# Optimization experiments

Measured on AMD Instinct MI355X. Metric: run time of the kernel, lower is better.

Reference implementation:

```python
import jax, jax.numpy as jnp
import numpy as np

WS = 7      # window size
SHIFT = 3   # shift size
H = 56
W = 56
NH = 16     # num heads


def _layernorm(x, g, b):
    m = x.mean(-1, keepdims=True)
    v = x.var(-1, keepdims=True)
    return (x - m) / jnp.sqrt(v + 1e-5) * g + b


def setup_inputs() -> dict:
    key = jax.random.key(0)
    ks = jax.random.split(key, 8)
    B, C = 16, 512
    DH = 4 * C
    s = 0.02
    x = jax.random.normal(ks[0], (B, H * W, C), jnp.float32)

    # relative position index (matches torch buffer construction)
    coords = np.stack(np.meshgrid(np.arange(WS), np.arange(WS), indexing='ij')).reshape(2, -1)
    rel = (coords[:, :, None] - coords[:, None, :]).transpose(1, 2, 0).copy()
    rel[..., 0] += WS - 1
    rel[..., 1] += WS - 1
    rel[..., 0] *= 2 * WS - 1
    rpi = jnp.asarray(rel.sum(-1), jnp.int32)  # (49, 49)

    # shifted-window additive attention mask (nW, N, N)
    img = np.zeros((H, W))
    cnt = 0
    for hs in (slice(0, -WS), slice(-WS, -SHIFT), slice(-SHIFT, None)):
        for wsl in (slice(0, -WS), slice(-WS, -SHIFT), slice(-SHIFT, None)):
            img[hs, wsl] = cnt
            cnt += 1
    mw = img.reshape(H // WS, WS, W // WS, WS).transpose(0, 2, 1, 3).reshape(-1, WS * WS)
    diff = mw[:, None, :] - mw[:, :, None]  # == mw.unsqueeze(1) - mw.unsqueeze(2)
    attn_mask = jnp.asarray(np.where(diff != 0, -100.0, 0.0), jnp.float32)

    return {
        'x': x,
        'rpi': rpi,
        'attn_mask': attn_mask,
        'norm1_g': jnp.ones((C,), jnp.float32),
        'norm1_b': jnp.zeros((C,), jnp.float32),
        'qkv_w': jax.random.normal(ks[1], (3 * C, C), jnp.float32) * s,
        'qkv_b': jnp.zeros((3 * C,), jnp.float32),
        'proj_w': jax.random.normal(ks[2], (C, C), jnp.float32) * s,
        'proj_b': jnp.zeros((C,), jnp.float32),
        'rpb_table': jax.random.normal(ks[3], ((2 * WS - 1) ** 2, NH), jnp.float32) * s,
        'norm2_g': jnp.ones((C,), jnp.float32),
        'norm2_b': jnp.zeros((C,), jnp.float32),
        'mlp_w1': jax.random.normal(ks[4], (DH, C), jnp.float32) * s,
        'mlp_b1': jnp.zeros((DH,), jnp.float32),
        'mlp_w2': jax.random.normal(ks[5], (C, DH), jnp.float32) * s,
        'mlp_b2': jnp.zeros((C,), jnp.float32),
    }


def reference(x, rpi, attn_mask, norm1_g, norm1_b, qkv_w, qkv_b, proj_w, proj_b,
              rpb_table, norm2_g, norm2_b, mlp_w1, mlp_b1, mlp_w2, mlp_b2):
    B, L, C = x.shape
    N = WS * WS
    nW = (H // WS) * (W // WS)
    hd = C // NH

    # --- attention branch ---
    h = _layernorm(x, norm1_g, norm1_b).reshape(B, H, W, C)
    h = jnp.roll(h, (-SHIFT, -SHIFT), axis=(1, 2))
    # window partition -> (B*nW, N, C)
    xw = h.reshape(B, H // WS, WS, W // WS, WS, C).transpose(0, 1, 3, 2, 4, 5).reshape(B * nW, N, C)

    qkv = (xw @ qkv_w.T + qkv_b).reshape(B * nW, N, 3, NH, hd).transpose(2, 0, 3, 1, 4)
    q, k, v = qkv[0], qkv[1], qkv[2]  # (B*nW, NH, N, hd)
    attn = jnp.einsum('bhnd,bhmd->bhnm', q * (hd ** -0.5), k)
    rpb = rpb_table[rpi].transpose(2, 0, 1)  # (NH, N, N)
    attn = attn + rpb[None]
    attn = attn.reshape(B, nW, NH, N, N) + attn_mask[None, :, None]
    attn = jax.nn.softmax(attn.reshape(B * nW, NH, N, N), axis=-1)
    o = jnp.einsum('bhnm,bhmd->bhnd', attn, v).transpose(0, 2, 1, 3).reshape(B * nW, N, C)
    o = o @ proj_w.T + proj_b
    # window reverse + unshift
    o = o.reshape(B, H // WS, W // WS, WS, WS, C).transpose(0, 1, 3, 2, 4, 5).reshape(B, H, W, C)
    o = jnp.roll(o, (SHIFT, SHIFT), axis=(1, 2)).reshape(B, L, C)

    x = x + o
    # --- MLP branch ---
    h2 = _layernorm(x, norm2_g, norm2_b)
    m = jax.nn.gelu(h2 @ mlp_w1.T + mlp_b1, approximate=False)
    return x + (m @ mlp_w2.T + mlp_b2)
```

## Files before the change

kernel.cpp:

```cpp
#include <hip/hip_runtime.h>
#include <hip/hip_bf16.h>

typedef __attribute__((ext_vector_type(8))) short bf16x8_t;
typedef __attribute__((ext_vector_type(4))) float f32x4_t;

__device__ __forceinline__ void gll16(const void* g, void* l) {
  __builtin_amdgcn_global_load_lds((const __attribute__((address_space(1))) void*)g,
                                   (__attribute__((address_space(3))) void*)l, 16, 0, 0);
}

__global__ __launch_bounds__(256) void k_cvt4(const float* __restrict__ s0, const float* __restrict__ s1,
                                              const float* __restrict__ s2, const float* __restrict__ s3,
                                              __hip_bfloat16* __restrict__ out) {
  int i4 = blockIdx.x * 256 + threadIdx.x;
  int i = i4 * 4;
  const float* src;
  int off;
  if (i < 786432)       { src = s0; off = i; }
  else if (i < 1048576) { src = s1; off = i - 786432; }
  else if (i < 2097152) { src = s2; off = i - 1048576; }
  else                  { src = s3; off = i - 2097152; }
  float4 v = *(const float4*)(src + off);
  union { __hip_bfloat16 h[4]; ushort2 u2[2]; } pk;
  pk.h[0] = __float2bfloat16(v.x); pk.h[1] = __float2bfloat16(v.y);
  pk.h[2] = __float2bfloat16(v.z); pk.h[3] = __float2bfloat16(v.w);
  *(ushort2*)(out + i) = pk.u2[0];
  *(ushort2*)(out + i + 2) = pk.u2[1];
}

__global__ __launch_bounds__(256) void k_cmb(const int* __restrict__ rpi,
                                             const float* __restrict__ tab,
                                             const float* __restrict__ mask,
                                             float* __restrict__ cmbp) {
  int idx = blockIdx.x * 256 + threadIdx.x;
  int jj = idx & 3, lane = (idx >> 2) & 63, tile = (idx >> 8) & 15;
  int h = (idx >> 12) & 15, w6 = idx >> 16;
  int r = (tile >> 2) * 16 + (lane >> 4) * 4 + jj;
  int c = (tile & 3) * 16 + (lane & 15);
  float v = -1e9f;
  if (r < 49 && c < 49) v = tab[rpi[r * 49 + c] * 16 + h] + mask[w6 * 2401 + r * 49 + c];
  cmbp[idx] = v;
}

template<int PERM>
__global__ __launch_bounds__(256) void k_ln(const float* __restrict__ in,
                                            const float* __restrict__ g,
                                            const float* __restrict__ bta,
                                            __hip_bfloat16* __restrict__ out) {
  const int w = threadIdx.x >> 6, l = threadIdx.x & 63;
  const int token = blockIdx.x * 4 + w;
  const float4* p = (const float4*)(in + (size_t)token * 512);
  float4 v0 = p[l], v1 = p[l + 64];
  float s  = v0.x + v0.y + v0.z + v0.w + v1.x + v1.y + v1.z + v1.w;
  float sq = v0.x*v0.x + v0.y*v0.y + v0.z*v0.z + v0.w*v0.w
           + v1.x*v1.x + v1.y*v1.y + v1.z*v1.z + v1.w*v1.w;
  #pragma unroll
  for (int d = 1; d < 64; d <<= 1) { s += __shfl_xor(s, d); sq += __shfl_xor(sq, d); }
  float mean = s * (1.f / 512.f);
  float inv = rsqrtf(sq * (1.f / 512.f) - mean * mean + 1e-5f);
  size_t dst;
  if (PERM) {
    int b = token / 3136, pp = token - b * 3136;
    int i = pp / 56, j = pp - i * 56;
    int gi = (i + 53) % 56, gj = (j + 53) % 56;
    dst = ((size_t)(((b * 64) + (gi / 7) * 8 + (gj / 7)) * 49) + (gi % 7) * 7 + (gj % 7)) * 512;
  } else {
    dst = (size_t)token * 512;
  }
  int c0 = l * 4, c1 = 256 + l * 4;
  union { __hip_bfloat16 h[4]; ushort4 u4; } a, b4;
  a.h[0] = __float2bfloat16((v0.x - mean) * inv * g[c0]     + bta[c0]);
  a.h[1] = __float2bfloat16((v0.y - mean) * inv * g[c0 + 1] + bta[c0 + 1]);
  a.h[2] = __float2bfloat16((v0.z - mean) * inv * g[c0 + 2] + bta[c0 + 2]);
  a.h[3] = __float2bfloat16((v0.w - mean) * inv * g[c0 + 3] + bta[c0 + 3]);
  b4.h[0] = __float2bfloat16((v1.x - mean) * inv * g[c1]     + bta[c1]);
  b4.h[1] = __float2bfloat16((v1.y - mean) * inv * g[c1 + 1] + bta[c1 + 1]);
  b4.h[2] = __float2bfloat16((v1.z - mean) * inv * g[c1 + 2] + bta[c1 + 2]);
  b4.h[3] = __float2bfloat16((v1.w - mean) * inv * g[c1 + 3] + bta[c1 + 3]);
  *(ushort4*)(out + dst + c0) = a.u4;
  *(ushort4*)(out + dst + c1) = b4.u4;
}

__global__ __launch_bounds__(256) void k_attn(const __hip_bfloat16* __restrict__ qkv,
                                              const float* __restrict__ cmbp,
                                              __hip_bfloat16* __restrict__ o) {
  __shared__ __align__(16) __hip_bfloat16 vt_all[4 * 32 * 72];
  __shared__ __align__(16) __hip_bfloat16 P_all[4 * 64 * 72];
  const int t = threadIdx.x, l = t & 63, w = t >> 6;
  const int bw = blockIdx.x;
  const int head = blockIdx.y * 4 + w;
  const int rr = l & 15, g = l >> 4;
  __hip_bfloat16* vt = vt_all + w * (32 * 72);
  __hip_bfloat16* P  = P_all  + w * (64 * 72);
  const __hip_bfloat16* base = qkv + (size_t)bw * 49 * 1536 + head * 32;
  const bf16x8_t zero8 = {};

  { int d = l >> 1, sg = (l & 1) * 8;
    *(bf16x8_t*)(vt + d * 72 + 48 + sg) = zero8; }
  __builtin_amdgcn_sched_barrier(0);
  #pragma unroll
  for (int it = 0; it < 4; ++it) {
    int idx = l + it * 64;
    if (idx < 196) {
      int j = idx >> 2, sg = (idx & 3) * 8;
      bf16x8_t vv = *(const bf16x8_t*)(base + 1024 + (size_t)j * 1536 + sg);
      #pragma unroll
      for (int s2 = 0; s2 < 8; ++s2) vt[(sg + s2) * 72 + j] = ((__hip_bfloat16*)&vv)[s2];
    }
  }
  bf16x8_t aq[4], bk[4];
  #pragma unroll
  for (int m = 0; m < 4; ++m) {
    int row = m * 16 + rr;
    aq[m] = (row < 49) ? *(const bf16x8_t*)(base + (size_t)row * 1536 + g * 8) : zero8;
    bk[m] = (row < 49) ? *(const bf16x8_t*)(base + 512 + (size_t)row * 1536 + g * 8) : zero8;
  }
  const float4* cp = (const float4*)(cmbp + (size_t)((bw & 63) * 16 + head) * 4096);
  f32x4_t S[4][4];
  #pragma unroll
  for (int tm = 0; tm < 4; ++tm)
    #pragma unroll
    for (int tn = 0; tn < 4; ++tn) {
      float4 cv = cp[(tm * 4 + tn) * 64 + l];
      f32x4_t c0 = { cv.x, cv.y, cv.z, cv.w };
      S[tm][tn] = __builtin_amdgcn_mfma_f32_16x16x32_bf16(aq[tm], bk[tn], c0, 0, 0, 0);
    }
  float sm[4][4];
  #pragma unroll
  for (int tm = 0; tm < 4; ++tm) {
    #pragma unroll
    for (int jj = 0; jj < 4; ++jj) {
      float v = fmaxf(fmaxf(S[tm][0][jj], S[tm][1][jj]), fmaxf(S[tm][2][jj], S[tm][3][jj]));
      v = fmaxf(v, __shfl_xor(v, 1));
      v = fmaxf(v, __shfl_xor(v, 2));
      v = fmaxf(v, __shfl_xor(v, 4));
      v = fmaxf(v, __shfl_xor(v, 8));
      float s = 0.f;
      #pragma unroll
      for (int tn = 0; tn < 4; ++tn) {
        float e = __expf(S[tm][tn][jj] - v);
        S[tm][tn][jj] = e;
        s += e;
      }
      s += __shfl_xor(s, 1); s += __shfl_xor(s, 2); s += __shfl_xor(s, 4); s += __shfl_xor(s, 8);
      sm[tm][jj] = s;
    }
  }
  #pragma unroll
  for (int tm = 0; tm < 4; ++tm)
    #pragma unroll
    for (int tn = 0; tn < 4; ++tn)
      #pragma unroll
      for (int jj = 0; jj < 4; ++jj)
        P[(tm * 16 + g * 4 + jj) * 72 + tn * 16 + rr] = __float2bfloat16(S[tm][tn][jj]);

  f32x4_t O[4][2] = {};
  #pragma unroll
  for (int ks = 0; ks < 2; ++ks) {
    bf16x8_t pa[4], vb[2];
    #pragma unroll
    for (int tm = 0; tm < 4; ++tm)
      pa[tm] = *(const bf16x8_t*)(P + (tm * 16 + rr) * 72 + ks * 32 + g * 8);
    #pragma unroll
    for (int tn = 0; tn < 2; ++tn)
      vb[tn] = *(const bf16x8_t*)(vt + (tn * 16 + rr) * 72 + ks * 32 + g * 8);
    #pragma unroll
    for (int tm = 0; tm < 4; ++tm)
      #pragma unroll
      for (int tn = 0; tn < 2; ++tn)
        O[tm][tn] = __builtin_amdgcn_mfma_f32_16x16x32_bf16(pa[tm], vb[tn], O[tm][tn], 0, 0, 0);
  }
  #pragma unroll
  for (int tm = 0; tm < 4; ++tm) {
    #pragma unroll
    for (int jj = 0; jj < 4; ++jj) {
      int r = tm * 16 + g * 4 + jj;
      if (r < 49) {
        float rcp = 1.f / sm[tm][jj];
        size_t ob = ((size_t)bw * 49 + r) * 512 + head * 32;
        o[ob + rr]      = __float2bfloat16(O[tm][0][jj] * rcp);
        o[ob + 16 + rr] = __float2bfloat16(O[tm][1][jj] * rcp);
      }
    }
  }
}

template<int EP>
__global__ __launch_bounds__(512, 2) void gemm256(const __hip_bfloat16* __restrict__ A,
                                                  const __hip_bfloat16* __restrict__ Bw,
                                                  int K, int Ncols, int nNB,
                                                  const float* __restrict__ bias,
                                                  __hip_bfloat16* __restrict__ obf,
                                                  const float* __restrict__ resid,
                                                  float* __restrict__ ofp) {
  __shared__ __align__(16) char LDS[131072];
  const int nwg = gridDim.x, orig = blockIdx.x;
  const int q8 = nwg >> 3, r8 = nwg & 7;
  const int xcd = orig & 7, lin = orig >> 3;
  const int wgid = (xcd < r8 ? xcd * (q8 + 1) : r8 * (q8 + 1) + (xcd - r8) * q8) + lin;
  const int bx = wgid / nNB, by = wgid - bx * nNB;
  const int m0 = bx * 256, n0 = by * 256;
  const int t = threadIdx.x, l = t & 63, w = t >> 6;
  const int wr = w >> 2, wc = w & 3;
  const int rr = l & 15, kq = l >> 4;
  const int swzo = (kq * 16) ^ ((rr & 8) << 2);

  int rs0, cs0, rs1, cs1;
  { int d = t * 16;  rs0 = (d >> 10) * 16 + ((d >> 6) & 15);
    cs0 = ((d & 63) ^ (((d >> 9) & 1) << 5)) >> 1; }
  { int d = 8192 + t * 16; int dd = d & 8191;
    rs1 = (dd >> 10) * 16 + ((dd >> 6) & 15);
    cs1 = 32 + (((d & 63) ^ (((d >> 9) & 1) << 5)) >> 1); }
  const __hip_bfloat16* gA = A + (size_t)m0 * K;
  const __hip_bfloat16* gB = Bw + (size_t)n0 * K;

  auto stageA = [&](int T, int h) {
    char* dst = LDS + (T & 1) * 32768 + h * 16384 + t * 16;
    const size_t kb = (size_t)T * 64;
    gll16(gA + (size_t)(h * 128 + rs0) * K + kb + cs0, dst);
    gll16(gA + (size_t)(h * 128 + rs1) * K + kb + cs1, dst + 8192);
  };
  auto stageB = [&](int T, int h) {
    char* dst = LDS + 65536 + (T & 1) * 32768 + h * 16384 + t * 16;
    const size_t kb = (size_t)T * 64;
    gll16(gB + (size_t)(h * 128 + rs0) * K + kb + cs0, dst);
    gll16(gB + (size_t)(h * 128 + rs1) * K + kb + cs1, dst + 8192);
  };

  auto ldA = [&](bf16x8_t (&a)[4][2], int buf, int mq) {
    const char* b = LDS + buf * 32768 + wr * 16384;
    #pragma unroll
    for (int m = 0; m < 4; ++m)
      #pragma unroll
      for (int ks = 0; ks < 2; ++ks)
        a[m][ks] = *(const bf16x8_t*)(b + ks * 8192 + (mq * 4 + m) * 1024 + rr * 64 + swzo);
  };
  auto ldB = [&](bf16x8_t (&bv)[2][2], int buf, int nq) {
    const char* b = LDS + 65536 + buf * 32768 + (wc >> 1) * 16384;
    #pragma unroll
    for (int n = 0; n < 2; ++n)
      #pragma unroll
      for (int ks = 0; ks < 2; ++ks)
        bv[n][ks] = *(const bf16x8_t*)(b + ks * 8192 + ((wc & 1) * 4 + nq * 2 + n) * 1024 + rr * 64 + swzo);
  };

  f32x4_t acc[8][4] = {};
  auto mma = [&](bf16x8_t (&a)[4][2], bf16x8_t (&bv)[2][2], int mq, int nq) {
    __builtin_amdgcn_s_setprio(1);
    #pragma unroll
    for (int m = 0; m < 4; ++m)
      #pragma unroll
      for (int n = 0; n < 2; ++n)
        #pragma unroll
        for (int ks = 0; ks < 2; ++ks)
          acc[mq * 4 + m][nq * 2 + n] =
            __builtin_amdgcn_mfma_f32_16x16x32_bf16(a[m][ks], bv[n][ks], acc[mq * 4 + m][nq * 2 + n], 0, 0, 0);
    __builtin_amdgcn_s_setprio(0);
  };

  const int NT = K >> 6;
  stageA(0, 0); stageB(0, 0); stageA(0, 1); stageB(0, 1);
  if (1 < NT) { stageA(1, 0); stageB(1, 0); }
  if (1 < NT) asm volatile("s_waitcnt vmcnt(4)" ::: "memory");
  else        asm volatile("s_waitcnt vmcnt(0)" ::: "memory");
  __builtin_amdgcn_s_barrier();

  for (int kt = 0; kt < NT; ++kt) {
    const int cur = kt & 1;
    bf16x8_t Alo[4][2], Ahi[4][2], B0[2][2], B1[2][2];
    ldA(Alo, cur, 0); ldB(B0, cur, 0);
    if (kt + 1 < NT) stageA(kt + 1, 1);
    mma(Alo, B0, 0, 0);
    ldA(Ahi, cur, 1);
    if (kt + 1 < NT) stageB(kt + 1, 1);
    mma(Ahi, B0, 1, 0);
    __builtin_amdgcn_s_barrier();
    ldB(B1, cur, 1);
    if (kt + 2 < NT) stageA(kt + 2, 0);
    mma(Ahi, B1, 1, 1);
    if (kt + 2 < NT) stageB(kt + 2, 0);
    mma(Alo, B1, 0, 1);
    if (kt + 1 < NT) {
      if (kt + 2 < NT) asm volatile("s_waitcnt vmcnt(4)" ::: "memory");
      else             asm volatile("s_waitcnt vmcnt(0)" ::: "memory");
    }
    __builtin_amdgcn_s_barrier();
  }

  #pragma unroll
  for (int m = 0; m < 8; ++m) {
    #pragma unroll
    for (int n = 0; n < 4; ++n) {
      const int gcol = n0 + wc * 64 + n * 16 + rr;
      #pragma unroll
      for (int j = 0; j < 4; ++j) {
        const int grow = m0 + wr * 128 + m * 16 + kq * 4 + j;
        float v = acc[m][n][j] + bias[gcol];
        if (EP == 0) {
          if (gcol < 512) v *= 0.17677669529663687f;
          obf[(size_t)grow * Ncols + gcol] = __float2bfloat16(v);
        } else if (EP == 1) {
          int bw = grow / 49, nn = grow - bw * 49;
          int b = bw >> 6, wi = bw & 63;
          int hh = (wi >> 3) * 7 + nn / 7 + 3;  if (hh >= 56) hh -= 56;
          int ww2 = (wi & 7) * 7 + (nn % 7) + 3; if (ww2 >= 56) ww2 -= 56;
          size_t tok = (size_t)b * 3136 + hh * 56 + ww2;
          ofp[tok * 512 + gcol] = resid[tok * 512 + gcol] + v;
        } else if (EP == 2) {
          float u = 0.5f * v * (1.f + erff(v * 0.70710678118f));
          obf[(size_t)grow * Ncols + gcol] = __float2bfloat16(u);
        } else {
          ofp[(size_t)grow * 512 + gcol] += v;
        }
      }
    }
  }
}

extern "C" void kernel_launch(void* const* d_in, const int* in_sizes, int n_in,
                              void* d_out, int out_size, void* d_ws, size_t ws_size,
                              hipStream_t stream) {
  const float* x      = (const float*)d_in[0];
  const int*   rpi    = (const int*)  d_in[1];
  const float* amask  = (const float*)d_in[2];
  const float* n1g    = (const float*)d_in[3];
  const float* n1b    = (const float*)d_in[4];
  const float* qkv_w  = (const float*)d_in[5];
  const float* qkv_b  = (const float*)d_in[6];
  const float* proj_w = (const float*)d_in[7];
  const float* proj_b = (const float*)d_in[8];
  const float* rpb_t  = (const float*)d_in[9];
  const float* n2g    = (const float*)d_in[10];
  const float* n2b    = (const float*)d_in[11];
  const float* w1     = (const float*)d_in[12];
  const float* b1     = (const float*)d_in[13];
  const float* w2     = (const float*)d_in[14];
  const float* b2     = (const float*)d_in[15];
  float* out = (float*)d_out;

  char* ws = (char*)d_ws;
  const size_t M = 50176;
  const size_t szA = M * 2048 * 2;
  const size_t szB = M * 1536 * 2;
  const size_t offB = szA;
  const size_t offW = offB + szB;
  __hip_bfloat16* bufA = (__hip_bfloat16*)(ws);
  __hip_bfloat16* bufB = (__hip_bfloat16*)(ws + offB);
  __hip_bfloat16* wqkv  = (__hip_bfloat16*)(ws + offW);
  float* cmbp = (float*)(ws + szA - (size_t)4194304 * 4);
  __hip_bfloat16* wproj = wqkv + 786432;
  __hip_bfloat16* wm1   = wproj + 262144;
  __hip_bfloat16* wm2   = wm1 + 1048576;

  k_cvt4<<<3072, 256, 0, stream>>>(qkv_w, proj_w, w1, w2, wqkv);
  k_cmb<<<16384, 256, 0, stream>>>(rpi, rpb_t, amask, cmbp);

  k_ln<1><<<12544, 256, 0, stream>>>(x, n1g, n1b, bufA);
  gemm256<0><<<196 * 6, 512, 0, stream>>>(bufA, wqkv, 512, 1536, 6, qkv_b, bufB, nullptr, nullptr);
  k_attn<<<dim3(1024, 4), 256, 0, stream>>>(bufB, cmbp, bufA);
  gemm256<1><<<196 * 2, 512, 0, stream>>>(bufA, wproj, 512, 512, 2, proj_b, nullptr, x, out);
  k_ln<0><<<12544, 256, 0, stream>>>(out, n2g, n2b, bufB);
  gemm256<2><<<196 * 8, 512, 0, stream>>>(bufB, wm1, 512, 2048, 8, b1, bufA, nullptr, nullptr);
  gemm256<3><<<196 * 2, 512, 0, stream>>>(bufA, wm2, 2048, 512, 2, b2, nullptr, nullptr, out);
}
```

Measured before the change: 761.9 us.

## Reshape GEMM tiles from 256x256 to 128x512 with a rebalanced staging schedule

Changes the GEMM block tile from 256x256 to 128 rows by 512 columns. Each of the eight waves now covers all 128 rows and a 64-column strip, and B is staged as four 128-row sub-tiles across a reworked double-buffered pipeline. For the N=512 projection and MLP-down GEMMs, a single column tile now covers the full output width, so A is read once and each row's epilogue index math (including the window-reverse scatter) is hoisted out of the column loop. In exchange, LDS grows to 160KB per block, which likely drops occupancy to one block per CU, and global load volume per output increases.

```diff
diff --git a/kernel.cpp b/kernel.cpp
--- a/kernel.cpp
+++ b/kernel.cpp
@@ -186,22 +186,21 @@
 }
 
 template<int EP>
-__global__ __launch_bounds__(512, 2) void gemm256(const __hip_bfloat16* __restrict__ A,
-                                                  const __hip_bfloat16* __restrict__ Bw,
-                                                  int K, int Ncols, int nNB,
-                                                  const float* __restrict__ bias,
-                                                  __hip_bfloat16* __restrict__ obf,
-                                                  const float* __restrict__ resid,
-                                                  float* __restrict__ ofp) {
-  __shared__ __align__(16) char LDS[131072];
+__global__ __launch_bounds__(512, 2) void gemm_w(const __hip_bfloat16* __restrict__ A,
+                                                 const __hip_bfloat16* __restrict__ Bw,
+                                                 int K, int Ncols, int nNB,
+                                                 const float* __restrict__ bias,
+                                                 __hip_bfloat16* __restrict__ obf,
+                                                 const float* __restrict__ resid,
+                                                 float* __restrict__ ofp) {
+  __shared__ __align__(16) char LDS[163840];
   const int nwg = gridDim.x, orig = blockIdx.x;
   const int q8 = nwg >> 3, r8 = nwg & 7;
   const int xcd = orig & 7, lin = orig >> 3;
   const int wgid = (xcd < r8 ? xcd * (q8 + 1) : r8 * (q8 + 1) + (xcd - r8) * q8) + lin;
   const int bx = wgid / nNB, by = wgid - bx * nNB;
-  const int m0 = bx * 256, n0 = by * 256;
+  const int m0 = bx * 128, n0 = by * 512;
   const int t = threadIdx.x, l = t & 63, w = t >> 6;
-  const int wr = w >> 2, wc = w & 3;
   const int rr = l & 15, kq = l >> 4;
   const int swzo = (kq * 16) ^ ((rr & 8) << 2);
 
@@ -214,34 +213,39 @@
   const __hip_bfloat16* gA = A + (size_t)m0 * K;
   const __hip_bfloat16* gB = Bw + (size_t)n0 * K;
 
-  auto stageA = [&](int T, int h) {
-    char* dst = LDS + (T & 1) * 32768 + h * 16384 + t * 16;
+  auto stageA = [&](int T) {
+    char* dst = LDS + (T & 1) * 16384 + t * 16;
     const size_t kb = (size_t)T * 64;
-    gll16(gA + (size_t)(h * 128 + rs0) * K + kb + cs0, dst);
-    gll16(gA + (size_t)(h * 128 + rs1) * K + kb + cs1, dst + 8192);
-  };
-  auto stageB = [&](int T, int h) {
-    char* dst = LDS + 65536 + (T & 1) * 32768 + h * 16384 + t * 16;
+    gll16(gA + (size_t)rs0 * K + kb + cs0, dst);
+    gll16(gA + (size_t)rs1 * K + kb + cs1, dst + 8192);
+  };
+  auto stageBu = [&](int T, int u) {
+    char* dst = LDS + 32768 + (T & 1) * 65536 + u * 16384 + t * 16;
     const size_t kb = (size_t)T * 64;
-    gll16(gB + (size_t)(h * 128 + rs0) * K + kb + cs0, dst);
-    gll16(gB + (size_t)(h * 128 + rs1) * K + kb + cs1, dst + 8192);
+    gll16(gB + (size_t)(u * 128 + rs0) * K + kb + cs0, dst);
+    gll16(gB + (size_t)(u * 128 + rs1) * K + kb + cs1, dst + 8192);
   };
 
   auto ldA = [&](bf16x8_t (&a)[4][2], int buf, int mq) {
-    const char* b = LDS + buf * 32768 + wr * 16384;
-    #pragma unroll
-    for (int m = 0; m < 4; ++m)
+    const char* b = LDS + buf * 16384;
+    #pragma unroll
+    for (int m = 0; m < 4; ++m) {
+      int r = mq * 64 + m * 16 + rr;
       #pragma unroll
       for (int ks = 0; ks < 2; ++ks)
-        a[m][ks] = *(const bf16x8_t*)(b + ks * 8192 + (mq * 4 + m) * 1024 + rr * 64 + swzo);
+        a[m][ks] = *(const bf16x8_t*)(b + ks * 8192 + (r >> 4) * 1024 + (r & 15) * 64 + swzo);
+    }
   };
   auto ldB = [&](bf16x8_t (&bv)[2][2], int buf, int nq) {
-    const char* b = LDS + 65536 + buf * 32768 + (wc >> 1) * 16384;
-    #pragma unroll
-    for (int n = 0; n < 2; ++n)
+    #pragma unroll
+    for (int n = 0; n < 2; ++n) {
+      int rB = w * 64 + (nq * 2 + n) * 16 + rr;
+      const char* b = LDS + 32768 + buf * 65536 + (rB >> 7) * 16384;
+      int r = rB & 127;
       #pragma unroll
       for (int ks = 0; ks < 2; ++ks)
-        bv[n][ks] = *(const bf16x8_t*)(b + ks * 8192 + ((wc & 1) * 4 + nq * 2 + n) * 1024 + rr * 64 + swzo);
+        bv[n][ks] = *(const bf16x8_t*)(b + ks * 8192 + (r >> 4) * 1024 + (r & 15) * 64 + swzo);
+    }
   };
 
   f32x4_t acc[8][4] = {};
@@ -259,30 +263,31 @@
   };
 
   const int NT = K >> 6;
-  stageA(0, 0); stageB(0, 0); stageA(0, 1); stageB(0, 1);
-  if (1 < NT) { stageA(1, 0); stageB(1, 0); }
+  stageA(0); stageBu(0, 0); stageBu(0, 1); stageBu(0, 2); stageBu(0, 3);
+  if (1 < NT) { stageBu(1, 0); stageBu(1, 1); }
   if (1 < NT) asm volatile("s_waitcnt vmcnt(4)" ::: "memory");
   else        asm volatile("s_waitcnt vmcnt(0)" ::: "memory");
   __builtin_amdgcn_s_barrier();
 
   for (int kt = 0; kt < NT; ++kt) {
     const int cur = kt & 1;
-    bf16x8_t Alo[4][2], Ahi[4][2], B0[2][2], B1[2][2];
-    ldA(Alo, cur, 0); ldB(B0, cur, 0);
-    if (kt + 1 < NT) stageA(kt + 1, 1);
-    mma(Alo, B0, 0, 0);
-    ldA(Ahi, cur, 1);
-    if (kt + 1 < NT) stageB(kt + 1, 1);
-    mma(Ahi, B0, 1, 0);
+    const bool nx1 = (kt + 1 < NT), nx2 = (kt + 2 < NT);
+    bf16x8_t Am0[4][2], Am1[4][2], Bn0[2][2], Bn1[2][2];
+    ldA(Am0, cur, 0); ldB(Bn0, cur, 0);
+    if (nx1) stageBu(kt + 1, 2);
+    mma(Am0, Bn0, 0, 0);
+    ldA(Am1, cur, 1); ldB(Bn1, cur, 1);
+    if (nx1) stageBu(kt + 1, 3);
+    mma(Am1, Bn0, 1, 0);
     __builtin_amdgcn_s_barrier();
-    ldB(B1, cur, 1);
-    if (kt + 2 < NT) stageA(kt + 2, 0);
-    mma(Ahi, B1, 1, 1);
-    if (kt + 2 < NT) stageB(kt + 2, 0);
-    mma(Alo, B1, 0, 1);
-    if (kt + 1 < NT) {
-      if (kt + 2 < NT) asm volatile("s_waitcnt vmcnt(4)" ::: "memory");
-      else             asm volatile("s_waitcnt vmcnt(0)" ::: "memory");
+    if (nx1) stageA(kt + 1);
+    if (nx2) stageBu(kt + 2, 0);
+    mma(Am1, Bn1, 1, 1);
+    if (nx2) stageBu(kt + 2, 1);
+    mma(Am0, Bn1, 0, 1);
+    if (nx1) {
+      if (nx2) asm volatile("s_waitcnt vmcnt(4)" ::: "memory");
+      else     asm volatile("s_waitcnt vmcnt(0)" ::: "memory");
     }
     __builtin_amdgcn_s_barrier();
   }
@@ -290,27 +295,34 @@
   #pragma unroll
   for (int m = 0; m < 8; ++m) {
     #pragma unroll
-    for (int n = 0; n < 4; ++n) {
-      const int gcol = n0 + wc * 64 + n * 16 + rr;
-      #pragma unroll
-      for (int j = 0; j < 4; ++j) {
-        const int grow = m0 + wr * 128 + m * 16 + kq * 4 + j;
+    for (int j = 0; j < 4; ++j) {
+      const int grow = m0 + m * 16 + kq * 4 + j;
+      size_t rowbase;
+      if (EP == 1) {
+        int bw = grow / 49, nn = grow - bw * 49;
+        int b = bw >> 6, wi = bw & 63;
+        int hh = (wi >> 3) * 7 + nn / 7 + 3;  if (hh >= 56) hh -= 56;
+        int ww2 = (wi & 7) * 7 + (nn % 7) + 3; if (ww2 >= 56) ww2 -= 56;
+        rowbase = ((size_t)b * 3136 + hh * 56 + ww2) * 512;
+      } else if (EP == 3) {
+        rowbase = (size_t)grow * 512;
+      } else {
+        rowbase = (size_t)grow * Ncols;
+      }
+      #pragma unroll
+      for (int n = 0; n < 4; ++n) {
+        const int gcol = n0 + w * 64 + n * 16 + rr;
         float v = acc[m][n][j] + bias[gcol];
         if (EP == 0) {
           if (gcol < 512) v *= 0.17677669529663687f;
-          obf[(size_t)grow * Ncols + gcol] = __float2bfloat16(v);
+          obf[rowbase + gcol] = __float2bfloat16(v);
         } else if (EP == 1) {
-          int bw = grow / 49, nn = grow - bw * 49;
-          int b = bw >> 6, wi = bw & 63;
-          int hh = (wi >> 3) * 7 + nn / 7 + 3;  if (hh >= 56) hh -= 56;
-          int ww2 = (wi & 7) * 7 + (nn % 7) + 3; if (ww2 >= 56) ww2 -= 56;
-          size_t tok = (size_t)b * 3136 + hh * 56 + ww2;
-          ofp[tok * 512 + gcol] = resid[tok * 512 + gcol] + v;
+          ofp[rowbase + gcol] = resid[rowbase + gcol] + v;
         } else if (EP == 2) {
           float u = 0.5f * v * (1.f + erff(v * 0.70710678118f));
-          obf[(size_t)grow * Ncols + gcol] = __float2bfloat16(u);
+          obf[rowbase + gcol] = __float2bfloat16(u);
         } else {
-          ofp[(size_t)grow * 512 + gcol] += v;
+          ofp[rowbase + gcol] += v;
         }
       }
     }
@@ -356,10 +368,10 @@
   k_cmb<<<16384, 256, 0, stream>>>(rpi, rpb_t, amask, cmbp);
 
   k_ln<1><<<12544, 256, 0, stream>>>(x, n1g, n1b, bufA);
-  gemm256<0><<<196 * 6, 512, 0, stream>>>(bufA, wqkv, 512, 1536, 6, qkv_b, bufB, nullptr, nullptr);
+  gemm_w<0><<<392 * 3, 512, 0, stream>>>(bufA, wqkv, 512, 1536, 3, qkv_b, bufB, nullptr, nullptr);
   k_attn<<<dim3(1024, 4), 256, 0, stream>>>(bufB, cmbp, bufA);
-  gemm256<1><<<196 * 2, 512, 0, stream>>>(bufA, wproj, 512, 512, 2, proj_b, nullptr, x, out);
+  gemm_w<1><<<392, 512, 0, stream>>>(bufA, wproj, 512, 512, 1, proj_b, nullptr, x, out);
   k_ln<0><<<12544, 256, 0, stream>>>(out, n2g, n2b, bufB);
-  gemm256<2><<<196 * 8, 512, 0, stream>>>(bufB, wm1, 512, 2048, 8, b1, bufA, nullptr, nullptr);
-  gemm256<3><<<196 * 2, 512, 0, stream>>>(bufA, wm2, 2048, 512, 2, b2, nullptr, nullptr, out);
-}
+  gemm_w<2><<<392 * 4, 512, 0, stream>>>(bufB, wm1, 512, 2048, 4, b1, bufA, nullptr, nullptr);
+  gemm_w<3><<<392, 512, 0, stream>>>(bufA, wm2, 2048, 512, 1, b2, nullptr, nullptr, out);
+}
```

New measurement: 777.6 us. 2.1% more time.

## Fuse projection GEMM with residual and LayerNorm2; split-K the second MLP GEMM

Applied to the files above, without the earlier changes.

A new kernel computes full 128x512 row tiles of the attention projection. In its epilogue it un-permutes rows back to token order, adds the residual, writes the fp32 output and applies LayerNorm2 to produce the bf16 MLP input. This removes the separate LayerNorm kernel and its extra pass over the activations. The final MLP GEMM is also split along K into two halves that atomically add into the output, doubling the number of workgroups for the 392-tile problem. The costs are a heavier epilogue with 160KB of LDS per block, which limits occupancy, plus fp32 atomic traffic and non-deterministic summation order.

```diff
diff --git a/kernel.cpp b/kernel.cpp
--- a/kernel.cpp
+++ b/kernel.cpp
@@ -42,11 +42,10 @@
   cmbp[idx] = v;
 }
 
-template<int PERM>
-__global__ __launch_bounds__(256) void k_ln(const float* __restrict__ in,
-                                            const float* __restrict__ g,
-                                            const float* __restrict__ bta,
-                                            __hip_bfloat16* __restrict__ out) {
+__global__ __launch_bounds__(256) void k_ln1(const float* __restrict__ in,
+                                             const float* __restrict__ g,
+                                             const float* __restrict__ bta,
+                                             __hip_bfloat16* __restrict__ out) {
   const int w = threadIdx.x >> 6, l = threadIdx.x & 63;
   const int token = blockIdx.x * 4 + w;
   const float4* p = (const float4*)(in + (size_t)token * 512);
@@ -58,15 +57,10 @@
   for (int d = 1; d < 64; d <<= 1) { s += __shfl_xor(s, d); sq += __shfl_xor(sq, d); }
   float mean = s * (1.f / 512.f);
   float inv = rsqrtf(sq * (1.f / 512.f) - mean * mean + 1e-5f);
-  size_t dst;
-  if (PERM) {
-    int b = token / 3136, pp = token - b * 3136;
-    int i = pp / 56, j = pp - i * 56;
-    int gi = (i + 53) % 56, gj = (j + 53) % 56;
-    dst = ((size_t)(((b * 64) + (gi / 7) * 8 + (gj / 7)) * 49) + (gi % 7) * 7 + (gj % 7)) * 512;
-  } else {
-    dst = (size_t)token * 512;
-  }
+  int b = token / 3136, pp = token - b * 3136;
+  int i = pp / 56, j = pp - i * 56;
+  int gi = (i + 53) % 56, gj = (j + 53) % 56;
+  size_t dst = ((size_t)(((b * 64) + (gi / 7) * 8 + (gj / 7)) * 49) + (gi % 7) * 7 + (gj % 7)) * 512;
   int c0 = l * 4, c1 = 256 + l * 4;
   union { __hip_bfloat16 h[4]; ushort4 u4; } a, b4;
   a.h[0] = __float2bfloat16((v0.x - mean) * inv * g[c0]     + bta[c0]);
@@ -188,17 +182,18 @@
 template<int EP>
 __global__ __launch_bounds__(512, 2) void gemm256(const __hip_bfloat16* __restrict__ A,
                                                   const __hip_bfloat16* __restrict__ Bw,
-                                                  int K, int Ncols, int nNB,
+                                                  int K, int Ncols, int nNB, int nMN, int NTp,
                                                   const float* __restrict__ bias,
                                                   __hip_bfloat16* __restrict__ obf,
-                                                  const float* __restrict__ resid,
                                                   float* __restrict__ ofp) {
   __shared__ __align__(16) char LDS[131072];
   const int nwg = gridDim.x, orig = blockIdx.x;
   const int q8 = nwg >> 3, r8 = nwg & 7;
   const int xcd = orig & 7, lin = orig >> 3;
   const int wgid = (xcd < r8 ? xcd * (q8 + 1) : r8 * (q8 + 1) + (xcd - r8) * q8) + lin;
-  const int bx = wgid / nNB, by = wgid - bx * nNB;
+  const int kz = wgid / nMN, rem = wgid - kz * nMN;
+  const int bx = rem / nNB, by = rem - bx * nNB;
+  const int koff = kz * NTp * 64;
   const int m0 = bx * 256, n0 = by * 256;
   const int t = threadIdx.x, l = t & 63, w = t >> 6;
   const int wr = w >> 2, wc = w & 3;
@@ -216,13 +211,13 @@
 
   auto stageA = [&](int T, int h) {
     char* dst = LDS + (T & 1) * 32768 + h * 16384 + t * 16;
-    const size_t kb = (size_t)T * 64;
+    const size_t kb = (size_t)T * 64 + koff;
     gll16(gA + (size_t)(h * 128 + rs0) * K + kb + cs0, dst);
     gll16(gA + (size_t)(h * 128 + rs1) * K + kb + cs1, dst + 8192);
   };
   auto stageB = [&](int T, int h) {
     char* dst = LDS + 65536 + (T & 1) * 32768 + h * 16384 + t * 16;
-    const size_t kb = (size_t)T * 64;
+    const size_t kb = (size_t)T * 64 + koff;
     gll16(gB + (size_t)(h * 128 + rs0) * K + kb + cs0, dst);
     gll16(gB + (size_t)(h * 128 + rs1) * K + kb + cs1, dst + 8192);
   };
@@ -258,7 +253,7 @@
     __builtin_amdgcn_s_setprio(0);
   };
 
-  const int NT = K >> 6;
+  const int NT = NTp;
   stageA(0, 0); stageB(0, 0); stageA(0, 1); stageB(0, 1);
   if (1 < NT) { stageA(1, 0); stageB(1, 0); }
   if (1 < NT) asm volatile("s_waitcnt vmcnt(4)" ::: "memory");
@@ -295,23 +290,184 @@
       #pragma unroll
       for (int j = 0; j < 4; ++j) {
         const int grow = m0 + wr * 128 + m * 16 + kq * 4 + j;
-        float v = acc[m][n][j] + bias[gcol];
+        float v = acc[m][n][j];
         if (EP == 0) {
+          v += bias[gcol];
           if (gcol < 512) v *= 0.17677669529663687f;
           obf[(size_t)grow * Ncols + gcol] = __float2bfloat16(v);
-        } else if (EP == 1) {
-          int bw = grow / 49, nn = grow - bw * 49;
-          int b = bw >> 6, wi = bw & 63;
-          int hh = (wi >> 3) * 7 + nn / 7 + 3;  if (hh >= 56) hh -= 56;
-          int ww2 = (wi & 7) * 7 + (nn % 7) + 3; if (ww2 >= 56) ww2 -= 56;
-          size_t tok = (size_t)b * 3136 + hh * 56 + ww2;
-          ofp[tok * 512 + gcol] = resid[tok * 512 + gcol] + v;
         } else if (EP == 2) {
+          v += bias[gcol];
           float u = 0.5f * v * (1.f + erff(v * 0.70710678118f));
           obf[(size_t)grow * Ncols + gcol] = __float2bfloat16(u);
         } else {
-          ofp[(size_t)grow * 512 + gcol] += v;
+          if (koff == 0) v += bias[gcol];
+          atomicAdd(ofp + (size_t)grow * 512 + gcol, v);
         }
+      }
+    }
+  }
+}
+
+__global__ __launch_bounds__(512, 2) void k_proj_ln(const __hip_bfloat16* __restrict__ A,
+                                                    const __hip_bfloat16* __restrict__ Bw,
+                                                    const float* __restrict__ bias,
+                                                    const float* __restrict__ resid,
+                                                    float* __restrict__ ofp,
+                                                    const float* __restrict__ g2,
+                                                    const float* __restrict__ b2,
+                                                    __hip_bfloat16* __restrict__ obf) {
+  const int K = 512;
+  __shared__ __align__(16) char LDS[163840];
+  const int nwg = gridDim.x, orig = blockIdx.x;
+  const int q8 = nwg >> 3, r8 = nwg & 7;
+  const int xcd = orig & 7, lin = orig >> 3;
+  const int wgid = (xcd < r8 ? xcd * (q8 + 1) : r8 * (q8 + 1) + (xcd - r8) * q8) + lin;
+  const int m0 = wgid * 128;
+  const int t = threadIdx.x, l = t & 63, w = t >> 6;
+  const int rr = l & 15, kq = l >> 4;
+  const int swzo = (kq * 16) ^ ((rr & 8) << 2);
+
+  int rs0, cs0, rs1, cs1;
+  { int d = t * 16;  rs0 = (d >> 10) * 16 + ((d >> 6) & 15);
+    cs0 = ((d & 63) ^ (((d >> 9) & 1) << 5)) >> 1; }
+  { int d = 8192 + t * 16; int dd = d & 8191;
+    rs1 = (dd >> 10) * 16 + ((dd >> 6) & 15);
+    cs1 = 32 + (((d & 63) ^ (((d >> 9) & 1) << 5)) >> 1); }
+  const __hip_bfloat16* gA = A + (size_t)m0 * K;
+  const __hip_bfloat16* gB = Bw;
+
+  auto stageA = [&](int T) {
+    char* dst = LDS + (T & 1) * 16384 + t * 16;
+    const size_t kb = (size_t)T * 64;
+    gll16(gA + (size_t)rs0 * K + kb + cs0, dst);
+    gll16(gA + (size_t)rs1 * K + kb + cs1, dst + 8192);
+  };
+  auto stageBu = [&](int T, int u) {
+    char* dst = LDS + 32768 + (T & 1) * 65536 + u * 16384 + t * 16;
+    const size_t kb = (size_t)T * 64;
+    gll16(gB + (size_t)(u * 128 + rs0) * K + kb + cs0, dst);
+    gll16(gB + (size_t)(u * 128 + rs1) * K + kb + cs1, dst + 8192);
+  };
+  auto ldA = [&](bf16x8_t (&a)[4][2], int buf, int mq) {
+    const char* b = LDS + buf * 16384;
+    #pragma unroll
+    for (int m = 0; m < 4; ++m) {
+      int r = mq * 64 + m * 16 + rr;
+      #pragma unroll
+      for (int ks = 0; ks < 2; ++ks)
+        a[m][ks] = *(const bf16x8_t*)(b + ks * 8192 + (r >> 4) * 1024 + (r & 15) * 64 + swzo);
+    }
+  };
+  auto ldB = [&](bf16x8_t (&bv)[2][2], int buf, int nq) {
+    #pragma unroll
+    for (int n = 0; n < 2; ++n) {
+      int rB = w * 64 + (nq * 2 + n) * 16 + rr;
+      const char* b = LDS + 32768 + buf * 65536 + (rB >> 7) * 16384;
+      int r = rB & 127;
+      #pragma unroll
+      for (int ks = 0; ks < 2; ++ks)
+        bv[n][ks] = *(const bf16x8_t*)(b + ks * 8192 + (r >> 4) * 1024 + (r & 15) * 64 + swzo);
+    }
+  };
+
+  f32x4_t acc[8][4] = {};
+  auto mma = [&](bf16x8_t (&a)[4][2], bf16x8_t (&bv)[2][2], int mq, int nq) {
+    __builtin_amdgcn_s_setprio(1);
+    #pragma unroll
+    for (int m = 0; m < 4; ++m)
+      #pragma unroll
+      for (int n = 0; n < 2; ++n)
+        #pragma unroll
+        for (int ks = 0; ks < 2; ++ks)
+          acc[mq * 4 + m][nq * 2 + n] =
+            __builtin_amdgcn_mfma_f32_16x16x32_bf16(a[m][ks], bv[n][ks], acc[mq * 4 + m][nq * 2 + n], 0, 0, 0);
+    __builtin_amdgcn_s_setprio(0);
+  };
+
+  const int NT = K >> 6;
+  stageA(0); stageBu(0, 0); stageBu(0, 1); stageBu(0, 2); stageBu(0, 3);
+  stageBu(1, 0); stageBu(1, 1);
+  asm volatile("s_waitcnt vmcnt(4)" ::: "memory");
+  __builtin_amdgcn_s_barrier();
+
+  for (int kt = 0; kt < NT; ++kt) {
+    const int cur = kt & 1;
+    const bool nx1 = (kt + 1 < NT), nx2 = (kt + 2 < NT);
+    bf16x8_t Am0[4][2], Am1[4][2], Bn0[2][2], Bn1[2][2];
+    ldA(Am0, cur, 0); ldB(Bn0, cur, 0);
+    if (nx1) stageBu(kt + 1, 2);
+    mma(Am0, Bn0, 0, 0);
+    ldA(Am1, cur, 1); ldB(Bn1, cur, 1);
+    if (nx1) stageBu(kt + 1, 3);
+    mma(Am1, Bn0, 1, 0);
+    __builtin_amdgcn_s_barrier();
+    if (nx1) stageA(kt + 1);
+    if (nx2) stageBu(kt + 2, 0);
+    mma(Am1, Bn1, 1, 1);
+    if (nx2) stageBu(kt + 2, 1);
+    mma(Am0, Bn1, 0, 1);
+    if (nx1) {
+      if (nx2) asm volatile("s_waitcnt vmcnt(4)" ::: "memory");
+      else     asm volatile("s_waitcnt vmcnt(0)" ::: "memory");
+    }
+    __builtin_amdgcn_s_barrier();
+  }
+
+  float* rsums = (float*)LDS;
+  float* rqs   = rsums + 1024;
+  float* rmean = rqs + 1024;
+  float* rinv  = rmean + 128;
+  size_t rowbase[8][4];
+  #pragma unroll
+  for (int m = 0; m < 8; ++m) {
+    #pragma unroll
+    for (int j = 0; j < 4; ++j) {
+      const int grow = m0 + m * 16 + kq * 4 + j;
+      int bw = grow / 49, nn = grow - bw * 49;
+      int b = bw >> 6, wi = bw & 63;
+      int hh = (wi >> 3) * 7 + nn / 7 + 3;  if (hh >= 56) hh -= 56;
+      int ww2 = (wi & 7) * 7 + (nn % 7) + 3; if (ww2 >= 56) ww2 -= 56;
+      rowbase[m][j] = ((size_t)b * 3136 + hh * 56 + ww2) * 512;
+      float s = 0.f, q = 0.f;
+      #pragma unroll
+      for (int n = 0; n < 4; ++n) {
+        const int gcol = w * 64 + n * 16 + rr;
+        float o = resid[rowbase[m][j] + gcol] + acc[m][n][j] + bias[gcol];
+        ofp[rowbase[m][j] + gcol] = o;
+        acc[m][n][j] = o;
+        s += o; q += o * o;
+      }
+      s += __shfl_xor(s, 1); q += __shfl_xor(q, 1);
+      s += __shfl_xor(s, 2); q += __shfl_xor(q, 2);
+      s += __shfl_xor(s, 4); q += __shfl_xor(q, 4);
+      s += __shfl_xor(s, 8); q += __shfl_xor(q, 8);
+      if (rr == 0) {
+        int row = m * 16 + kq * 4 + j;
+        rsums[row * 8 + w] = s; rqs[row * 8 + w] = q;
+      }
+    }
+  }
+  __syncthreads();
+  if (t < 128) {
+    float s = 0.f, q = 0.f;
+    #pragma unroll
+    for (int wv = 0; wv < 8; ++wv) { s += rsums[t * 8 + wv]; q += rqs[t * 8 + wv]; }
+    float mean = s * (1.f / 512.f);
+    rmean[t] = mean;
+    rinv[t] = rsqrtf(q * (1.f / 512.f) - mean * mean + 1e-5f);
+  }
+  __syncthreads();
+  #pragma unroll
+  for (int m = 0; m < 8; ++m) {
+    #pragma unroll
+    for (int j = 0; j < 4; ++j) {
+      int row = m * 16 + kq * 4 + j;
+      float mean = rmean[row], inv = rinv[row];
+      #pragma unroll
+      for (int n = 0; n < 4; ++n) {
+        const int gcol = w * 64 + n * 16 + rr;
+        float h = (acc[m][n][j] - mean) * inv * g2[gcol] + b2[gcol];
+        obf[rowbase[m][j] + gcol] = __float2bfloat16(h);
       }
     }
   }
@@ -355,11 +511,10 @@
   k_cvt4<<<3072, 256, 0, stream>>>(qkv_w, proj_w, w1, w2, wqkv);
   k_cmb<<<16384, 256, 0, stream>>>(rpi, rpb_t, amask, cmbp);
 
-  k_ln<1><<<12544, 256, 0, stream>>>(x, n1g, n1b, bufA);
-  gemm256<0><<<196 * 6, 512, 0, stream>>>(bufA, wqkv, 512, 1536, 6, qkv_b, bufB, nullptr, nullptr);
+  k_ln1<<<12544, 256, 0, stream>>>(x, n1g, n1b, bufA);
+  gemm256<0><<<1176, 512, 0, stream>>>(bufA, wqkv, 512, 1536, 6, 1176, 8, qkv_b, bufB, nullptr);
   k_attn<<<dim3(1024, 4), 256, 0, stream>>>(bufB, cmbp, bufA);
-  gemm256<1><<<196 * 2, 512, 0, stream>>>(bufA, wproj, 512, 512, 2, proj_b, nullptr, x, out);
-  k_ln<0><<<12544, 256, 0, stream>>>(out, n2g, n2b, bufB);
-  gemm256<2><<<196 * 8, 512, 0, stream>>>(bufB, wm1, 512, 2048, 8, b1, bufA, nullptr, nullptr);
-  gemm256<3><<<196 * 2, 512, 0, stream>>>(bufA, wm2, 2048, 512, 2, b2, nullptr, nullptr, out);
-}
+  k_proj_ln<<<392, 512, 0, stream>>>(bufA, wproj, proj_b, x, out, n2g, n2b, bufB);
+  gemm256<2><<<1568, 512, 0, stream>>>(bufB, wm1, 512, 2048, 8, 1568, 8, b1, bufA, nullptr);
+  gemm256<4><<<784, 512, 0, stream>>>(bufA, wm2, 2048, 512, 2, 392, 16, b2, nullptr, out);
+}
```

After: 995.5 us. +30.7%, slower.
